# Performance work log

Hardware: AMD Instinct MI355X
Metric: run time of the kernel (lower is better)

Reference implementation:

```python
import jax, jax.numpy as jnp
import numpy as np

B, T, D, V, U = 16, 1000, 512, 5000, 64


def _safe_logaddexp(a, b):
    # logaddexp with nan-safe gradients when both args are -inf
    both = jnp.isneginf(a) & jnp.isneginf(b)
    a_ = jnp.where(both, 0.0, a)
    b_ = jnp.where(both, 0.0, b)
    return jnp.where(both, -jnp.inf, jnp.logaddexp(a_, b_))


def _log_sub_exp(a, b):
    # faithful port of log_substraction_exp: log(exp(a) - exp(b)), stable
    mask1 = (~jnp.isinf(a)) & (~jnp.isinf(b))
    a_ = jnp.where(mask1, a, -1.0)
    b_ = jnp.where(mask1, b, -2.0)
    ans_tmp = b_ + jnp.log(jnp.exp(a_ - b_) - 1.0)
    a_ = jnp.where(jnp.isinf(ans_tmp), -2000.0, a_)
    b_ = jnp.where(jnp.isinf(ans_tmp), -2001.0, b_)
    ans1 = b_ + jnp.log(jnp.exp(a_ - b_) - 1.0)
    ans = jnp.where(mask1, ans1, -jnp.inf)
    mask2 = (~jnp.isinf(a)) & jnp.isinf(b)
    return jnp.where(mask2, a, ans)


def _ctc_trellis(logp, ys):
    # Standard CTC lattice over extended labels (blank interleaved), S = 2U+1.
    # alpha[t,b,s]: logprob of paths over frames 0..t ending in state s (incl. emission at t)
    # beta[t,b,s]:  logprob of emitting frames t+1..T-1 and finishing, given state s at t
    # This reproduces the k2 lattice forward/backward scores at the label states.
    Bb, Tt, _ = logp.shape
    Uu = ys.shape[1]
    S = 2 * Uu + 1
    l_ext = jnp.zeros((Bb, S), ys.dtype).at[:, 1::2].set(ys)  # blank=0 at even s
    lp = jnp.take_along_axis(logp, jnp.broadcast_to(l_ext[:, None, :], (Bb, Tt, S)), axis=2)
    skip_ok = jnp.zeros((Bb, S), bool).at[:, 3::2].set(ys[:, 1:] != ys[:, :-1])
    lpT = jnp.transpose(lp, (1, 0, 2))  # [T,B,S]
    ninf1 = jnp.full((Bb, 1), -jnp.inf)
    ninf2 = jnp.full((Bb, 2), -jnp.inf)

    a0 = jnp.full((Bb, S), -jnp.inf).at[:, :2].set(lpT[0, :, :2])

    def astep(ap, lp_t):
        s1 = jnp.concatenate([ninf1, ap[:, :-1]], 1)
        s2 = jnp.concatenate([ninf2, ap[:, :-2]], 1)
        a = lp_t + _safe_logaddexp(_safe_logaddexp(ap, s1), jnp.where(skip_ok, s2, -jnp.inf))
        return a, a

    _, arest = jax.lax.scan(astep, a0, lpT[1:])
    alpha = jnp.concatenate([a0[None], arest], 0)  # [T,B,S]

    bl = jnp.full((Bb, S), -jnp.inf).at[:, S - 2:].set(0.0)  # final states: last label / last blank
    skipL2 = jnp.concatenate([skip_ok[:, 2:], jnp.zeros((Bb, 2), bool)], 1)

    def bstep(bn, lp_next):
        m = lp_next + bn
        m1 = jnp.concatenate([m[:, 1:], ninf1], 1)
        m2 = jnp.concatenate([m[:, 2:], ninf2], 1)
        bcur = _safe_logaddexp(_safe_logaddexp(m, m1), jnp.where(skipL2, m2, -jnp.inf))
        return bcur, bcur

    _, brest = jax.lax.scan(bstep, bl, lpT[1:], reverse=True)
    beta = jnp.concatenate([brest, bl[None]], 0)  # [T,B,S]
    return alpha, beta, lp


def setup_inputs() -> dict:
    key = jax.random.key(0)
    k1, k2, k3 = jax.random.split(key, 3)
    hs_pad = jax.random.normal(k1, (B, T, D), jnp.float32)
    hlens = jnp.full((B,), T, jnp.int32)
    ys_pad = jax.random.randint(k2, (B, U), 1, V)  # labels in [1, V); 0 is blank
    ali = jnp.zeros((B, U), jnp.int32)  # unused when risk_factor == 0
    W = jax.random.normal(k3, (D, V), jnp.float32) * 0.02
    b = jnp.zeros((V,), jnp.float32)
    return {"hs_pad": hs_pad, "hlens": hlens, "ys_pad": ys_pad, "ali": ali, "W": W, "b": b}


def reference(hs_pad, hlens, ys_pad, ali, W, b):
    # ctc_lo + log_softmax (dropout_rate=0). hlens are all equal -> sort/unsort is identity.
    logp = jax.nn.log_softmax(hs_pad @ W + b, axis=-1)  # [B,T,V]
    alpha_f, beta_f, lp = _ctc_trellis(logp, ys_pad)
    alpha = jnp.transpose(alpha_f[:, :, 1::2], (1, 2, 0))  # [B,U,T]
    beta = jnp.transpose(beta_f[:, :, 1::2], (1, 2, 0))    # [B,U,T]
    p = jnp.transpose(lp[:, :, 1::2], (0, 2, 1))           # [B,U,T] logprob of label u at frame t
    # beta', excluding re-emission of label u at t+1 -> paths whose label-u segment ends at t
    bp = _log_sub_exp(beta[:, :, :-1], beta[:, :, 1:] + p[:, :, 1:])
    bp = jnp.concatenate([bp, beta[:, :, -1:]], -1)
    loss_state = alpha + bp
    loss_state = jnp.where(jnp.isnan(loss_state), -jnp.inf, loss_state)
    loss_u = jax.nn.logsumexp(loss_state, axis=2)  # aggregate == 'time'
    mask = jnp.isinf(loss_u)
    denom = (~mask).astype(loss_u.dtype).sum(1)
    loss_fsas = jnp.where(mask, 0.0, loss_u).sum(1) / denom
    Uu = ys_pad.shape[1]
    loss_fsas = jnp.where(hlens < Uu, 0.0, loss_fsas)
    return (-loss_fsas).mean()
```

## Files before the change

kernel.cpp:

```cpp
#include <hip/hip_runtime.h>

#define NB 16
#define NT 1000
#define ND 512
#define NV 5000
#define NVP 5120
#define NU 64
#define NLL 66
#define NM (NB * NT)
#define NCH 40

typedef short short8v __attribute__((ext_vector_type(8)));
typedef float float4v __attribute__((ext_vector_type(4)));

#define NEGINF (-__builtin_inff())
#define SENTL  (-1.0e30f)
#define LOG2E 1.4426950408889634f
#define LN2F  0.6931471805599453f
#define SENT2 (-2000.4586751f * LOG2E)

__device__ __forceinline__ float fexp2(float x) { return __builtin_amdgcn_exp2f(x); }
__device__ __forceinline__ float flog2(float x) { return __builtin_amdgcn_logf(x); }

__device__ __forceinline__ float dpp_shl1(float x) {
  int xi = __builtin_bit_cast(int, x);
  int r = __builtin_amdgcn_update_dpp(xi, xi, 0x130, 0xf, 0xf, false);
  return __builtin_bit_cast(float, r);
}
__device__ __forceinline__ float dpp_shr1(float x) {
  int xi = __builtin_bit_cast(int, x);
  int r = __builtin_amdgcn_update_dpp(xi, xi, 0x138, 0xf, 0xf, false);
  return __builtin_bit_cast(float, r);
}

__device__ __forceinline__ short f2bf(float x) {
  unsigned int u = __builtin_bit_cast(unsigned int, x);
  unsigned int r = (u + 0x7fffu + ((u >> 16) & 1u)) >> 16;
  return (short)(unsigned short)r;
}
__device__ __forceinline__ float bf2f(short h) {
  unsigned int u = ((unsigned int)(unsigned short)h) << 16;
  return __builtin_bit_cast(float, u);
}

__device__ __forceinline__ void g2lds16(const short* g, short* l) {
  __builtin_amdgcn_global_load_lds(
      (const __attribute__((address_space(1))) void*)g,
      (__attribute__((address_space(3))) void*)l, 16, 0, 0);
}

__device__ __forceinline__ float lae2s(float a, float b) {
  float m = fmaxf(a, b);
  return m + flog2(fexp2(a - m) + fexp2(b - m));
}
__device__ __forceinline__ float lae3s(float a, float b, float c) {
  float m = fmaxf(fmaxf(a, b), c);
  return m + flog2(fexp2(a - m) + fexp2(b - m) + fexp2(c - m));
}
__device__ __forceinline__ float lsub2(float a, float b) {
  if (b < -1.0e29f) return (a < -1.0e29f) ? SENTL : a;
  float tmp = b + flog2(fexp2(a - b) - 1.0f);
  if (__builtin_isinf(tmp)) tmp = SENT2;
  return tmp;
}

__global__ __launch_bounds__(256) void k_cvt(const float* __restrict__ hs,
                                             const float* __restrict__ W,
                                             short* __restrict__ hsb,
                                             short* __restrict__ WT,
                                             short* __restrict__ WTlo,
                                             float* __restrict__ outv) {
  __shared__ short tileH[64 * 72];
  __shared__ short tileL[64 * 72];
  if (blockIdx.x < 4000) {
    if (blockIdx.x == 0 && threadIdx.x == 0) outv[0] = 0.0f;
    size_t i = (size_t)blockIdx.x * 256 + threadIdx.x;
    const float4* p = (const float4*)hs + i * 2;
    float4 v0 = p[0], v1 = p[1];
    short8v r;
    r[0] = f2bf(v0.x); r[1] = f2bf(v0.y); r[2] = f2bf(v0.z); r[3] = f2bf(v0.w);
    r[4] = f2bf(v1.x); r[5] = f2bf(v1.y); r[6] = f2bf(v1.z); r[7] = f2bf(v1.w);
    int row = (int)(i >> 6);
    int g = (int)(i & 63);
    int gs = (g & ~7) | ((g & 7) ^ (row & 7));
    *(short8v*)(hsb + (size_t)row * ND + gs * 8) = r;
    return;
  }
  int bx = blockIdx.x - 4000;
  int n0 = (bx % 80) * 64, k0 = (bx / 80) * 64;
  int tid = threadIdx.x;
  int kr = tid >> 2, part = tid & 3;
  const float* src = W + (size_t)(k0 + kr) * NV + n0 + part * 16;
#pragma unroll
  for (int jj = 0; jj < 4; ++jj) {
    int c = n0 + part * 16 + jj * 4;
    float4 v;
    if (c + 3 < NV) {
      v = *(const float4*)(src + jj * 4);
    } else {
      v.x = (c + 0 < NV) ? src[jj * 4 + 0] : 0.f;
      v.y = (c + 1 < NV) ? src[jj * 4 + 1] : 0.f;
      v.z = (c + 2 < NV) ? src[jj * 4 + 2] : 0.f;
      v.w = (c + 3 < NV) ? src[jj * 4 + 3] : 0.f;
    }
    int base = kr * 72 + part * 16 + jj * 4;
    float vv[4] = {v.x, v.y, v.z, v.w};
#pragma unroll
    for (int q = 0; q < 4; ++q) {
      short h = f2bf(vv[q]);
      tileH[base + q] = h;
      tileL[base + q] = f2bf(vv[q] - bf2f(h));
    }
  }
  __syncthreads();
  int n = tid & 63, kq = tid >> 6;
  int nn = n0 + n;
  if (nn < NVP) {
#pragma unroll
    for (int half = 0; half < 2; ++half) {
      short8v vh, vl;
#pragma unroll
      for (int jj = 0; jj < 8; ++jj) {
        vh[jj] = tileH[(kq * 16 + half * 8 + jj) * 72 + n];
        vl[jj] = tileL[(kq * 16 + half * 8 + jj) * 72 + n];
      }
      int g = (k0 >> 3) + kq * 2 + half;
      int gs = (g & ~7) | ((g & 7) ^ (nn & 7));
      *(short8v*)(WT + (size_t)nn * ND + gs * 8) = vh;
      *(short8v*)(WTlo + (size_t)nn * ND + gs * 8) = vl;
    }
  }
}

__global__ __launch_bounds__(256) void k_labg(const short* __restrict__ hsb,
                                              const short* __restrict__ WT,
                                              const short* __restrict__ WTlo,
                                              const int* __restrict__ ys,
                                              const float* __restrict__ bias,
                                              float* __restrict__ ll) {
  __shared__ short As[128 * 64];
  __shared__ short Bh[128 * 64];
  __shared__ short Bl[128 * 64];

  int mt = blockIdx.x, b = blockIdx.y;
  int t0 = mt * 128;
  int tid = threadIdx.x;
  int lane = tid & 63, wave = tid >> 6;
  int wm = wave >> 1, wn = wave & 1;
  int lrow = lane & 15, lkhi = lane >> 4;

  const short* gaBase = hsb + (size_t)(b * NT + t0 + wave * 32 + (lane >> 3)) * ND + (lane & 7) * 8;

  int labv[4], xorv[4];
#pragma unroll
  for (int i = 0; i < 4; ++i) {
    int r = wave * 32 + (lane >> 3) + i * 8;
    int lab = (r == 0) ? 0 : ((r <= NU) ? ys[b * NU + r - 1] : NV);
    labv[i] = lab;
    xorv[i] = ((lane & 7) ^ (r & 7) ^ (lab & 7)) * 8;
  }

  float4v acc[4][4];
#pragma unroll
  for (int m = 0; m < 4; ++m)
#pragma unroll
    for (int n = 0; n < 4; ++n)
#pragma unroll
      for (int j = 0; j < 4; ++j) acc[m][n][j] = 0.f;

  for (int s = 0; s < 8; ++s) {
    int k0 = s * 64;
#pragma unroll
    for (int i = 0; i < 4; ++i) {
      g2lds16(gaBase + (size_t)(i * 8) * ND + k0, &As[(wave * 32 + i * 8) * 64]);
      g2lds16(WT + (size_t)labv[i] * ND + k0 + xorv[i], &Bh[(wave * 32 + i * 8) * 64]);
      g2lds16(WTlo + (size_t)labv[i] * ND + k0 + xorv[i], &Bl[(wave * 32 + i * 8) * 64]);
    }
    __syncthreads();
#pragma unroll
    for (int kk = 0; kk < 2; ++kk) {
      short8v av[4], bhv[4], blv2[4];
#pragma unroll
      for (int m = 0; m < 4; ++m) {
        int r = wm * 64 + m * 16 + lrow;
        int col = (kk * 32 + lkhi * 8) ^ ((r & 7) << 3);
        av[m] = *(const short8v*)&As[r * 64 + col];
      }
#pragma unroll
      for (int n = 0; n < 4; ++n) {
        int r = wn * 64 + n * 16 + lrow;
        int col = (kk * 32 + lkhi * 8) ^ ((r & 7) << 3);
        bhv[n] = *(const short8v*)&Bh[r * 64 + col];
        blv2[n] = *(const short8v*)&Bl[r * 64 + col];
      }
#pragma unroll
      for (int m = 0; m < 4; ++m)
#pragma unroll
        for (int n = 0; n < 4; ++n) {
          acc[m][n] = __builtin_amdgcn_mfma_f32_16x16x32_bf16(av[m], bhv[n], acc[m][n], 0, 0, 0);
          acc[m][n] = __builtin_amdgcn_mfma_f32_16x16x32_bf16(av[m], blv2[n], acc[m][n], 0, 0, 0);
        }
    }
    __syncthreads();
  }

  float bu[4]; bool uval[4];
#pragma unroll
  for (int n = 0; n < 4; ++n) {
    int u = wn * 64 + n * 16 + lrow;
    uval[n] = u < NU + 1;
    int lab = (u == 0) ? 0 : (uval[n] ? ys[b * NU + u - 1] : 0);
    bu[n] = uval[n] ? bias[lab] : 0.f;
  }
#pragma unroll
  for (int m = 0; m < 4; ++m)
#pragma unroll
    for (int j = 0; j < 4; ++j) {
      int trow = t0 + wm * 64 + m * 16 + lkhi * 4 + j;
      if (trow < NT) {
#pragma unroll
        for (int n = 0; n < 4; ++n) {
          int u = wn * 64 + n * 16 + lrow;
          if (uval[n])
            ll[((size_t)(b * NLL + u)) * NT + trow] = acc[m][n][j] + bu[n];
        }
      }
    }
}

__global__ __launch_bounds__(256) void k_big(const short* __restrict__ hsb,
                                             const short* __restrict__ WT,
                                             const float* __restrict__ bias,
                                             const float* __restrict__ ll,
                                             const int* __restrict__ ys,
                                             float* __restrict__ L,
                                             float* __restrict__ aod) {
  __shared__ short As[2][128 * 64];
  __shared__ short Ws[2][128 * 64];
  __shared__ float mred[128][2];
  __shared__ float sred[128][2];

  int bid = blockIdx.x;
  int tid = threadIdx.x;

  if (bid < NB) {
    float* pbS = (float*)As;
    int b = bid;
    const float* llb = ll + (size_t)b * NLL * NT;
    for (int i = tid; i < NT; i += 256) pbS[i] = llb[i] * LOG2E;
    __syncthreads();
    if (tid >= 64) return;
    int l = tid;
    const float* lrow = llb + (size_t)(1 + l) * NT;

    int lab = ys[b * NU + l];
    int labp = ys[b * NU + ((l >= 1) ? (l - 1) : 0)];
    bool skip = (l >= 1) && (lab != labp);
    float* aodb = aod + (size_t)b * NT * NU;

    float ae = (l == 0) ? pbS[0] : SENTL;
    float ao = (l == 0) ? lrow[0] * LOG2E : SENTL;
    aodb[l] = ao;

    float cl[16], pbr[16];
#pragma unroll
    for (int j = 0; j < 16; ++j) {
      int tt = 1 + j; if (tt > NT - 1) tt = NT - 1;
      cl[j] = lrow[tt];
      pbr[j] = pbS[tt];
    }
    for (int g = 0; g < 63; ++g) {
      float nl[16], pb2[16];
      if (g < 62) {
#pragma unroll
        for (int j = 0; j < 16; ++j) {
          int tt = 17 + g * 16 + j; if (tt > NT - 1) tt = NT - 1;
          nl[j] = lrow[tt];
          pb2[j] = pbS[tt];
        }
      } else {
#pragma unroll
        for (int j = 0; j < 16; ++j) { nl[j] = 0.f; pb2[j] = 0.f; }
      }
#pragma unroll
      for (int j = 0; j < 16; ++j) {
        int t = 1 + g * 16 + j;
        if (t < NT) {
          float pb = pbr[j];
          float pl = cl[j] * LOG2E;
          float po = dpp_shr1(ao); if (l == 0) po = SENTL;
          float aen = pb + lae2s(ae, po);
          float aon = pl + lae3s(ao, ae, skip ? po : SENTL);
          ae = aen; ao = aon;
          aodb[t * NU + l] = ao;
        }
      }
#pragma unroll
      for (int j = 0; j < 16; ++j) { cl[j] = nl[j]; pbr[j] = pb2[j]; }
    }
    return;
  }

  int lin = bid - NB;
  int o = (lin & 7) * 625 + (lin >> 3);
  int mt, chunk;
  if (o < 4800) {
    int sb = o / 320, w = o % 320;
    mt = sb * 8 + (w & 7);
    chunk = w >> 3;
  } else {
    int w = o - 4800;
    mt = 120 + (w % 5);
    chunk = w / 5;
  }
  int t0 = mt * 128;
  int n0 = chunk * 128;
  int lane = tid & 63, wave = tid >> 6;
  int wm = wave >> 1, wn = wave & 1;
  int lrow = lane & 15, lkhi = lane >> 4;

  const short* gaBase = hsb + (size_t)(t0 + wave * 32 + (lane >> 3)) * ND + (lane & 7) * 8;
  const short* gwBase = WT + (size_t)(n0 + wave * 32 + (lane >> 3)) * ND + (lane & 7) * 8;

  float4v acc[4][4];
#pragma unroll
  for (int m = 0; m < 4; ++m)
#pragma unroll
    for (int n = 0; n < 4; ++n)
#pragma unroll
      for (int j = 0; j < 4; ++j) acc[m][n][j] = 0.f;

  auto stage = [&](int s, int bw) {
    int k0 = s * 64;
#pragma unroll
    for (int i = 0; i < 4; ++i) {
      g2lds16(gaBase + (size_t)(i * 8) * ND + k0, &As[bw][(wave * 32 + i * 8) * 64]);
      g2lds16(gwBase + (size_t)(i * 8) * ND + k0, &Ws[bw][(wave * 32 + i * 8) * 64]);
    }
  };
  auto compute = [&](int bw) {
#pragma unroll
    for (int kk = 0; kk < 2; ++kk) {
      short8v av[4], wv[4];
#pragma unroll
      for (int m = 0; m < 4; ++m) {
        int r = wm * 64 + m * 16 + lrow;
        int col = (kk * 32 + lkhi * 8) ^ ((r & 7) << 3);
        av[m] = *(const short8v*)&As[bw][r * 64 + col];
      }
#pragma unroll
      for (int n = 0; n < 4; ++n) {
        int r = wn * 64 + n * 16 + lrow;
        int col = (kk * 32 + lkhi * 8) ^ ((r & 7) << 3);
        wv[n] = *(const short8v*)&Ws[bw][r * 64 + col];
      }
#pragma unroll
      for (int m = 0; m < 4; ++m)
#pragma unroll
        for (int n = 0; n < 4; ++n)
          acc[m][n] = __builtin_amdgcn_mfma_f32_16x16x32_bf16(av[m], wv[n], acc[m][n], 0, 0, 0);
    }
  };

  stage(0, 0);
  for (int s = 0; s < 8; ++s) {
    if (s < 7) {
      stage(s + 1, (s + 1) & 1);
      asm volatile("s_waitcnt vmcnt(8)" ::: "memory");
    } else {
      asm volatile("s_waitcnt vmcnt(0)" ::: "memory");
    }
    __builtin_amdgcn_sched_barrier(0);
    __builtin_amdgcn_s_barrier();
    compute(s & 1);
    __builtin_amdgcn_sched_barrier(0);
    __builtin_amdgcn_s_barrier();
  }

  float bcol[4]; bool cval[4];
#pragma unroll
  for (int n = 0; n < 4; ++n) {
    int c = n0 + wn * 64 + n * 16 + lrow;
    cval[n] = c < NV;
    bcol[n] = cval[n] ? bias[c] : 0.f;
  }
#pragma unroll
  for (int m = 0; m < 4; ++m)
#pragma unroll
    for (int j = 0; j < 4; ++j) {
      float mx = NEGINF;
#pragma unroll
      for (int n = 0; n < 4; ++n) {
        float v = cval[n] ? acc[m][n][j] + bcol[n] : NEGINF;
        mx = fmaxf(mx, v);
      }
#pragma unroll
      for (int d = 1; d < 16; d <<= 1) mx = fmaxf(mx, __shfl_xor(mx, d));
      float mxc = fmaxf(mx, -3.0e38f);
      float p = 0.f;
#pragma unroll
      for (int n = 0; n < 4; ++n) {
        float v = cval[n] ? acc[m][n][j] + bcol[n] : NEGINF;
        p += __expf(v - mxc);
      }
#pragma unroll
      for (int d = 1; d < 16; d <<= 1) p += __shfl_xor(p, d);
      if (lrow == 0) {
        int rloc = wm * 64 + m * 16 + lkhi * 4 + j;
        mred[rloc][wn] = mx;
        sred[rloc][wn] = p;
      }
    }
  __syncthreads();
  if (tid < 128) {
    int row = t0 + tid;
    float m0 = mred[tid][0], m1 = mred[tid][1];
    float m = fmaxf(m0, m1);
    float ss = 0.f;
    if (m != NEGINF)
      ss = ((m0 == NEGINF) ? 0.f : sred[tid][0] * __expf(m0 - m))
         + ((m1 == NEGINF) ? 0.f : sred[tid][1] * __expf(m1 - m));
    float Lv = (m == NEGINF || ss <= 0.f) ? NEGINF : m + __logf(ss);
    L[(size_t)chunk * NM + row] = Lv;
  }
}

__global__ __launch_bounds__(256) void k_dred(const float* __restrict__ L,
                                              float* __restrict__ dnm) {
  int row = blockIdx.x * 256 + threadIdx.x;
  if (row >= NM) return;
  float m40 = NEGINF;
#pragma unroll
  for (int c = 0; c < NCH; ++c) m40 = fmaxf(m40, L[(size_t)c * NM + row]);
  float s = 0.f;
#pragma unroll
  for (int c = 0; c < NCH; ++c) {
    float Lc = L[(size_t)c * NM + row];
    if (Lc > -1.0e29f) s += __expf(Lc - m40);
  }
  dnm[row] = m40 + __logf(s);
}

__global__ __launch_bounds__(256) void k_bwd(const float* __restrict__ ll,
                                             const float* __restrict__ dnm,
                                             const float* __restrict__ aod,
                                             const int* __restrict__ ys,
                                             const int* __restrict__ hlens,
                                             float* __restrict__ out) {
  __shared__ float dnS[NT];
  __shared__ float pbS[NT];
  __shared__ float Dpre[NT];
  __shared__ float choff[64];
  int b = blockIdx.x;
  int tid = threadIdx.x;
  const float* llb = ll + (size_t)b * NLL * NT;
  const float* dnb = dnm + b * NT;
  for (int t = tid; t < NT; t += 256) {
    float d = dnb[t];
    float blk = llb[t];
    dnS[t] = d;
    pbS[t] = (blk - d) * LOG2E;
  }
  __syncthreads();
  if (tid < 64) {
    float s = 0.f;
#pragma unroll
    for (int i = 0; i < 16; ++i) { int t = tid * 16 + i; if (t < NT) s += dnS[t]; }
    float v = s;
#pragma unroll
    for (int d = 1; d < 64; d <<= 1) { float u = __shfl_up(v, d); if (tid >= d) v += u; }
    choff[tid] = v - s;
  }
  __syncthreads();
  for (int t = tid; t < NT; t += 256) {
    float s = choff[t >> 4];
    int base = t & ~15;
    for (int i = base; i <= t; ++i) s += dnS[i];
    Dpre[t] = s;
  }
  __syncthreads();
  if (tid >= 64) return;
  int l = tid;
  const float* lrow = llb + (size_t)(1 + l) * NT;
  const float* ab = aod + (size_t)b * NT * NU;

  int lab = ys[b * NU + l];
  int labn = ys[b * NU + ((l < NU - 1) ? (l + 1) : l)];
  bool skipn = (l < NU - 1) && (labn != lab);

  float bo = (l == NU - 1) ? 0.0f : SENTL;
  float be = SENTL;
  float b128 = 0.0f;
  float mls = NEGINF, sls = 0.f;
  {
    float x = ab[(NT - 1) * NU + l] - Dpre[NT - 1] * LOG2E + bo;
    if (!(__builtin_isnan(x) || x < -1.0e29f)) { mls = x; sls = 1.0f; }
  }

  float cl[16], pbr[16], dnr[16], ba[16], dpr[16];
#pragma unroll
  for (int j = 0; j < 16; ++j) {
    int tt = NT - 2 - j; if (tt < 0) tt = 0;
    cl[j] = lrow[tt + 1];
    pbr[j] = pbS[tt + 1];
    dnr[j] = dnS[tt + 1];
    ba[j] = ab[tt * NU + l];
    dpr[j] = Dpre[tt];
  }
  for (int g = 0; g < 63; ++g) {
    float nl2[16], pb2[16], dn2[16], na[16], dp2[16];
    if (g < 62) {
#pragma unroll
      for (int j = 0; j < 16; ++j) {
        int tt = NT - 2 - 16 * (g + 1) - j; if (tt < 0) tt = 0;
        nl2[j] = lrow[tt + 1];
        pb2[j] = pbS[tt + 1];
        dn2[j] = dnS[tt + 1];
        na[j] = ab[tt * NU + l];
        dp2[j] = Dpre[tt];
      }
    } else {
#pragma unroll
      for (int j = 0; j < 16; ++j) { nl2[j] = 0.f; pb2[j] = 0.f; dn2[j] = 0.f; na[j] = 0.f; dp2[j] = 0.f; }
    }
#pragma unroll
    for (int j = 0; j < 16; ++j) {
      int t = NT - 2 - 16 * g - j;
      if (t >= 0) {
        float pbv = pbr[j];
        float plv = (cl[j] - dnr[j]) * LOG2E;
        float me = pbv + be;
        float mo = plv + bo;
        float m128 = pbv + b128;
        float ne = dpp_shl1(me); if (l == NU - 1) ne = m128;
        float no = dpp_shl1(mo); if (l == NU - 1) no = SENTL;
        float ben = lae2s(me, mo);
        float bon = lae3s(mo, ne, skipn ? no : SENTL);
        float pv = lsub2(bon, mo);
        float x = ba[j] - dpr[j] * LOG2E + pv;
        if (!(__builtin_isnan(x) || x < -1.0e29f)) {
          if (x > mls) { sls = sls * fexp2(mls - x) + 1.0f; mls = x; }
          else         { sls += fexp2(x - mls); }
        }
        be = ben; bo = bon; b128 = m128;
      }
    }
#pragma unroll
    for (int j = 0; j < 16; ++j) {
      cl[j] = nl2[j]; pbr[j] = pb2[j]; dnr[j] = dn2[j]; ba[j] = na[j]; dpr[j] = dp2[j];
    }
  }

  float lu = (mls == NEGINF) ? NEGINF : (mls + flog2(sls)) * LN2F;
  bool msk = __builtin_isinf(lu);
  float sv = msk ? 0.f : lu;
  float cv = msk ? 0.f : 1.f;
#pragma unroll
  for (int d = 1; d < 64; d <<= 1) { sv += __shfl_xor(sv, d); cv += __shfl_xor(cv, d); }
  if (l == 0) {
    float lf = sv / cv;
    if (hlens[b] < NU) lf = 0.f;
    atomicAdd(out, -lf * (1.0f / NB));
  }
}

extern "C" void kernel_launch(void* const* d_in, const int* in_sizes, int n_in,
                              void* d_out, int out_size, void* d_ws, size_t ws_size,
                              hipStream_t stream) {
  const float* hs    = (const float*)d_in[0];
  const int*   hlens = (const int*)d_in[1];
  const int*   ys    = (const int*)d_in[2];
  const float* W     = (const float*)d_in[4];
  const float* bias  = (const float*)d_in[5];
  float* out = (float*)d_out;

  char* ws = (char*)d_ws;
  short* hsb   = (short*)(ws + 0);
  short* WT    = (short*)(ws + 16384000);
  short* WTlo  = (short*)(ws + 21626880);
  float* aod   = (float*)(ws + 21626880);
  float* ll    = (float*)(ws + 26869760);
  float* L     = (float*)(ws + 31093760);
  float* dnm   = (float*)(ws + 33653760);

  k_cvt<<<4640, 256, 0, stream>>>(hs, W, hsb, WT, WTlo, out);
  k_labg<<<dim3(8, 16), 256, 0, stream>>>(hsb, WT, WTlo, ys, bias, ll);
  k_big<<<5016, 256, 0, stream>>>(hsb, WT, bias, ll, ys, L, aod);
  k_dred<<<63, 256, 0, stream>>>(L, dnm);
  k_bwd<<<NB, 256, 0, stream>>>(ll, dnm, aod, ys, hlens, out);
}
```

Measured before the change: 435.2 us.

## Split backward CTC recursion from loss reduction and parallelize time logsumexp

```diff
diff --git a/kernel.cpp b/kernel.cpp
--- a/kernel.cpp
+++ b/kernel.cpp
@@ -441,87 +441,56 @@
   dnm[row] = m40 + __logf(s);
 }
 
-__global__ __launch_bounds__(256) void k_bwd(const float* __restrict__ ll,
+__global__ __launch_bounds__(512) void k_bwd(const float* __restrict__ ll,
                                              const float* __restrict__ dnm,
-                                             const float* __restrict__ aod,
                                              const int* __restrict__ ys,
-                                             const int* __restrict__ hlens,
-                                             float* __restrict__ out) {
-  __shared__ float dnS[NT];
-  __shared__ float pbS[NT];
-  __shared__ float Dpre[NT];
-  __shared__ float choff[64];
-  int b = blockIdx.x;
-  int tid = threadIdx.x;
+                                             float* __restrict__ bp) {
+  __shared__ float dnS[8][NT];
+  __shared__ float pbS[8][NT];
+  int wave = threadIdx.x >> 6;
+  int l = threadIdx.x & 63;
+  int b = blockIdx.x * 8 + wave;
   const float* llb = ll + (size_t)b * NLL * NT;
   const float* dnb = dnm + b * NT;
-  for (int t = tid; t < NT; t += 256) {
+  for (int t = l; t < NT; t += 64) {
     float d = dnb[t];
-    float blk = llb[t];
-    dnS[t] = d;
-    pbS[t] = (blk - d) * LOG2E;
+    dnS[wave][t] = d;
+    pbS[wave][t] = (llb[t] - d) * LOG2E;
   }
   __syncthreads();
-  if (tid < 64) {
-    float s = 0.f;
-#pragma unroll
-    for (int i = 0; i < 16; ++i) { int t = tid * 16 + i; if (t < NT) s += dnS[t]; }
-    float v = s;
-#pragma unroll
-    for (int d = 1; d < 64; d <<= 1) { float u = __shfl_up(v, d); if (tid >= d) v += u; }
-    choff[tid] = v - s;
-  }
-  __syncthreads();
-  for (int t = tid; t < NT; t += 256) {
-    float s = choff[t >> 4];
-    int base = t & ~15;
-    for (int i = base; i <= t; ++i) s += dnS[i];
-    Dpre[t] = s;
-  }
-  __syncthreads();
-  if (tid >= 64) return;
-  int l = tid;
   const float* lrow = llb + (size_t)(1 + l) * NT;
-  const float* ab = aod + (size_t)b * NT * NU;
 
   int lab = ys[b * NU + l];
   int labn = ys[b * NU + ((l < NU - 1) ? (l + 1) : l)];
   bool skipn = (l < NU - 1) && (labn != lab);
+  float* bpb = bp + (size_t)b * NT * NU;
 
   float bo = (l == NU - 1) ? 0.0f : SENTL;
   float be = SENTL;
   float b128 = 0.0f;
-  float mls = NEGINF, sls = 0.f;
-  {
-    float x = ab[(NT - 1) * NU + l] - Dpre[NT - 1] * LOG2E + bo;
-    if (!(__builtin_isnan(x) || x < -1.0e29f)) { mls = x; sls = 1.0f; }
-  }
-
-  float cl[16], pbr[16], dnr[16], ba[16], dpr[16];
+  bpb[(NT - 1) * NU + l] = bo;
+
+  float cl[16], pbr[16], dnr[16];
 #pragma unroll
   for (int j = 0; j < 16; ++j) {
     int tt = NT - 2 - j; if (tt < 0) tt = 0;
     cl[j] = lrow[tt + 1];
-    pbr[j] = pbS[tt + 1];
-    dnr[j] = dnS[tt + 1];
-    ba[j] = ab[tt * NU + l];
-    dpr[j] = Dpre[tt];
+    pbr[j] = pbS[wave][tt + 1];
+    dnr[j] = dnS[wave][tt + 1];
   }
   for (int g = 0; g < 63; ++g) {
-    float nl2[16], pb2[16], dn2[16], na[16], dp2[16];
+    float nl2[16], pb2[16], dn2[16];
     if (g < 62) {
 #pragma unroll
       for (int j = 0; j < 16; ++j) {
         int tt = NT - 2 - 16 * (g + 1) - j; if (tt < 0) tt = 0;
         nl2[j] = lrow[tt + 1];
-        pb2[j] = pbS[tt + 1];
-        dn2[j] = dnS[tt + 1];
-        na[j] = ab[tt * NU + l];
-        dp2[j] = Dpre[tt];
+        pb2[j] = pbS[wave][tt + 1];
+        dn2[j] = dnS[wave][tt + 1];
       }
     } else {
 #pragma unroll
-      for (int j = 0; j < 16; ++j) { nl2[j] = 0.f; pb2[j] = 0.f; dn2[j] = 0.f; na[j] = 0.f; dp2[j] = 0.f; }
+      for (int j = 0; j < 16; ++j) { nl2[j] = 0.f; pb2[j] = 0.f; dn2[j] = 0.f; }
     }
 #pragma unroll
     for (int j = 0; j < 16; ++j) {
@@ -536,31 +505,82 @@
         float no = dpp_shl1(mo); if (l == NU - 1) no = SENTL;
         float ben = lae2s(me, mo);
         float bon = lae3s(mo, ne, skipn ? no : SENTL);
-        float pv = lsub2(bon, mo);
-        float x = ba[j] - dpr[j] * LOG2E + pv;
-        if (!(__builtin_isnan(x) || x < -1.0e29f)) {
-          if (x > mls) { sls = sls * fexp2(mls - x) + 1.0f; mls = x; }
-          else         { sls += fexp2(x - mls); }
-        }
+        bpb[t * NU + l] = lsub2(bon, mo);
         be = ben; bo = bon; b128 = m128;
       }
     }
 #pragma unroll
-    for (int j = 0; j < 16; ++j) {
-      cl[j] = nl2[j]; pbr[j] = pb2[j]; dnr[j] = dn2[j]; ba[j] = na[j]; dpr[j] = dp2[j];
-    }
-  }
-
-  float lu = (mls == NEGINF) ? NEGINF : (mls + flog2(sls)) * LN2F;
-  bool msk = __builtin_isinf(lu);
-  float sv = msk ? 0.f : lu;
-  float cv = msk ? 0.f : 1.f;
-#pragma unroll
-  for (int d = 1; d < 64; d <<= 1) { sv += __shfl_xor(sv, d); cv += __shfl_xor(cv, d); }
-  if (l == 0) {
-    float lf = sv / cv;
-    if (hlens[b] < NU) lf = 0.f;
-    atomicAdd(out, -lf * (1.0f / NB));
+    for (int j = 0; j < 16; ++j) { cl[j] = nl2[j]; pbr[j] = pb2[j]; dnr[j] = dn2[j]; }
+  }
+}
+
+__global__ __launch_bounds__(512) void k_loss(const float* __restrict__ aod,
+                                              const float* __restrict__ bp,
+                                              const float* __restrict__ dnm,
+                                              const int* __restrict__ hlens,
+                                              float* __restrict__ out) {
+  __shared__ float denL[NT];
+  __shared__ float Dpre[NT];
+  __shared__ float choff[64];
+  __shared__ float ms[8][64], ss[8][64];
+  int b = blockIdx.x, tid = threadIdx.x;
+  for (int t = tid; t < NT; t += 512) denL[t] = dnm[b * NT + t];
+  __syncthreads();
+  if (tid < 64) {
+    float s = 0.f;
+#pragma unroll
+    for (int i = 0; i < 16; ++i) { int t = tid * 16 + i; if (t < NT) s += denL[t]; }
+    float v = s;
+#pragma unroll
+    for (int d = 1; d < 64; d <<= 1) { float u = __shfl_up(v, d); if (tid >= d) v += u; }
+    choff[tid] = v - s;
+  }
+  __syncthreads();
+  for (int t = tid; t < NT; t += 512) {
+    float s = choff[t >> 4];
+    int base = t & ~15;
+    for (int i = base; i <= t; ++i) s += denL[i];
+    Dpre[t] = s;
+  }
+  __syncthreads();
+  int w = tid >> 6, l = tid & 63;
+  const float* ab = aod + (size_t)b * NT * NU;
+  const float* pbp = bp + (size_t)b * NT * NU;
+  float m = NEGINF, s = 0.f;
+  int t0 = w * 125, t1 = t0 + 125;
+  for (int t = t0; t < t1; ++t) {
+    float av = ab[t * NU + l];
+    float pv = pbp[t * NU + l];
+    float x = av - Dpre[t] * LOG2E + pv;
+    if (__builtin_isnan(x) || x < -1.0e29f) continue;
+    if (x > m) { s = s * fexp2(m - x) + 1.0f; m = x; }
+    else       { s += fexp2(x - m); }
+  }
+  ms[w][l] = m; ss[w][l] = s;
+  __syncthreads();
+  if (w == 0) {
+    float mm = NEGINF;
+#pragma unroll
+    for (int i = 0; i < 8; ++i) mm = fmaxf(mm, ms[i][l]);
+    float lu;
+    if (mm == NEGINF) lu = NEGINF;
+    else {
+      float st = 0.f;
+#pragma unroll
+      for (int i = 0; i < 8; ++i)
+        st += (ms[i][l] == NEGINF) ? 0.f : ss[i][l] * fexp2(ms[i][l] - mm);
+      lu = (mm + flog2(st)) * LN2F;
+    }
+    bool msk = __builtin_isinf(lu);
+    float sv = msk ? 0.f : lu;
+    float cv = msk ? 0.f : 1.f;
+#pragma unroll
+    for (int d = 1; d < 64; d <<= 1) { sv += __shfl_xor(sv, d); cv += __shfl_xor(cv, d); }
+    if (l == 0) {
+      float lf = sv / cv;
+      if (hlens[b] < NU) lf = 0.f;
+      atomicAdd(out, -lf * (1.0f / NB));
+    }
   }
 }
 
@@ -582,10 +602,12 @@
   float* ll    = (float*)(ws + 26869760);
   float* L     = (float*)(ws + 31093760);
   float* dnm   = (float*)(ws + 33653760);
+  float* bpb   = (float*)(ws + 33717760);
 
   k_cvt<<<4640, 256, 0, stream>>>(hs, W, hsb, WT, WTlo, out);
   k_labg<<<dim3(8, 16), 256, 0, stream>>>(hsb, WT, WTlo, ys, bias, ll);
   k_big<<<5016, 256, 0, stream>>>(hsb, WT, bias, ll, ys, L, aod);
   k_dred<<<63, 256, 0, stream>>>(L, dnm);
-  k_bwd<<<NB, 256, 0, stream>>>(ll, dnm, aod, ys, hlens, out);
-}
+  k_bwd<<<2, 512, 0, stream>>>(ll, dnm, ys, bpb);
+  k_loss<<<16, 512, 0, stream>>>(aod, bpb, dnm, hlens, out);
+}
```

Measured after the change: 447.5 us. 1.03x slower.
